# Performance work log

Measured on AMD Instinct MI355X. Metric: run time of the kernel, lower is better.

Reference implementation:

```python
import jax, jax.numpy as jnp
import numpy as np

L, H, E, DK, FF, V, BS = 6, 16, 1024, 64, 4096, 32000, 1024
B, T = 2, 1024
EPS = 1e-5


def _ln(x, g, b):
    mu = jnp.mean(x, axis=-1, keepdims=True)
    var = jnp.mean(jnp.square(x - mu), axis=-1, keepdims=True)
    return (x - mu) * jax.lax.rsqrt(var + EPS) * g + b


def setup_inputs() -> dict:
    key = jax.random.key(0)
    ks = jax.random.split(key, 12)
    s = 0.02
    return {
        'idx': jax.random.randint(ks[0], (B, T), 0, V),
        'emb': jax.random.normal(ks[1], (V, E), jnp.float32) * s,
        'pos': jax.random.normal(ks[2], (BS, E), jnp.float32) * s,
        'Wq': jax.random.normal(ks[3], (L, H, E, DK), jnp.float32) * s,
        'Wk': jax.random.normal(ks[4], (L, H, E, DK), jnp.float32) * s,
        'Wv': jax.random.normal(ks[5], (L, H, E, DK), jnp.float32) * s,
        'Wp': jax.random.normal(ks[6], (L, E, E), jnp.float32) * s,
        'bp': jnp.zeros((L, E), jnp.float32),
        'ln1_g': jnp.ones((L, E), jnp.float32),
        'ln1_b': jnp.zeros((L, E), jnp.float32),
        'ln2_g': jnp.ones((L, E), jnp.float32),
        'ln2_b': jnp.zeros((L, E), jnp.float32),
        'W1': jax.random.normal(ks[7], (L, E, FF), jnp.float32) * s,
        'b1': jnp.zeros((L, FF), jnp.float32),
        'W2': jax.random.normal(ks[8], (L, FF, E), jnp.float32) * s,
        'b2': jnp.zeros((L, E), jnp.float32),
        'lnf_g': jnp.ones((E,), jnp.float32),
        'lnf_b': jnp.zeros((E,), jnp.float32),
        'Wout': jax.random.normal(ks[9], (E, V), jnp.float32) * s,
        'bout': jnp.zeros((V,), jnp.float32),
    }


def reference(idx, emb, pos, Wq, Wk, Wv, Wp, bp, ln1_g, ln1_b, ln2_g, ln2_b,
              W1, b1, W2, b2, lnf_g, lnf_b, Wout, bout):
    Tcur = idx.shape[1]
    x = emb[idx] + pos[:Tcur]  # [B,T,E]
    # NOTE: original code scales by 1/sqrt(n_embd) (input dim), NOT 1/sqrt(d_k)
    scale = 1.0 / jnp.sqrt(jnp.float32(E))
    causal = jnp.tril(jnp.ones((Tcur, Tcur), bool))
    neg_inf = jnp.float32(-jnp.inf)
    for l in range(L):
        h = _ln(x, ln1_g[l], ln1_b[l])
        q = jnp.einsum('bte,hed->bhtd', h, Wq[l])
        k = jnp.einsum('bte,hed->bhtd', h, Wk[l])
        v = jnp.einsum('bte,hed->bhtd', h, Wv[l])
        scores = jnp.einsum('bhtd,bhsd->bhts', q, k) * scale
        scores = jnp.where(causal, scores, neg_inf)
        attn = jax.nn.softmax(scores, axis=-1)
        o = jnp.einsum('bhts,bhsd->bhtd', attn, v)
        o = o.transpose(0, 2, 1, 3).reshape(x.shape[0], Tcur, H * DK)
        x = x + o @ Wp[l] + bp[l]
        h = _ln(x, ln2_g[l], ln2_b[l])
        x = x + jax.nn.relu(h @ W1[l] + b1[l]) @ W2[l] + b2[l]
    x = _ln(x, lnf_g, lnf_b)
    logits = x @ Wout + bout  # [B,T,V]
    return logits
```

## Files before the change

### kernel.cpp

```cpp
#include <hip/hip_runtime.h>
#include <cstdio>
#include <cstdint>

typedef unsigned short u16;
typedef __bf16 bf16x8 __attribute__((ext_vector_type(8)));
typedef float f32x4 __attribute__((ext_vector_type(4)));

static const int EE = 1024;
static const int TT = 1024;
static const int BB = 2;
static const int NTOK = 2048;
static const int HH = 16;
static const int DK = 64;
static const int FF = 4096;
static const int VV = 32000;
static const int LL = 6;

__device__ __forceinline__ float bf2f(u16 u) {
  unsigned int i = ((unsigned int)u) << 16;
  float f; __builtin_memcpy(&f, &i, 4); return f;
}
__device__ __forceinline__ u16 f2bf(float f) {
  unsigned int i; __builtin_memcpy(&i, &f, 4);
  unsigned int r = i + 0x7fffu + ((i >> 16) & 1u);
  return (u16)(r >> 16);
}

__device__ __forceinline__ void gll16(const u16* g, u16* l) {
  __builtin_amdgcn_global_load_lds(
      (__attribute__((address_space(1))) void*)(uintptr_t)g,
      (__attribute__((address_space(3))) void*)l,
      16, 0, 0);
}

__global__ __launch_bounds__(256) void embed_k(const int* __restrict__ idx,
                                               const float* __restrict__ emb,
                                               const float* __restrict__ pos,
                                               float* __restrict__ x) {
  long i = (long)blockIdx.x * 256 + threadIdx.x;
  int n = (int)(i >> 10), e = (int)(i & 1023);
  int tok = idx[n];
  int t = n & (TT - 1);
  x[i] = emb[(long)tok * EE + e] + pos[(long)t * EE + e];
}

template <int NS>
__global__ __launch_bounds__(256) void ln_fused_k(float* __restrict__ x,
                                                  const float* __restrict__ part, long pstride,
                                                  const float* __restrict__ bias,
                                                  const float* __restrict__ g,
                                                  const float* __restrict__ b,
                                                  u16* __restrict__ out) {
  int row = blockIdx.x * 4 + (threadIdx.x >> 6);
  int lane = threadIdx.x & 63;
  long base = (long)row * EE;
  float v[16];
  float s = 0.f, s2 = 0.f;
#pragma unroll
  for (int j = 0; j < 16; j++) {
    int c = j * 64 + lane;
    float t = x[base + c];
    if constexpr (NS > 0) {
      t += bias[c];
#pragma unroll
      for (int p = 0; p < NS; p++) t += part[(long)p * pstride + base + c];
      x[base + c] = t;
    }
    v[j] = t; s += t; s2 += t * t;
  }
#pragma unroll
  for (int o = 32; o; o >>= 1) { s += __shfl_xor(s, o); s2 += __shfl_xor(s2, o); }
  float mu = s * (1.f / EE);
  float var = s2 * (1.f / EE) - mu * mu;
  float rs = rsqrtf(var + 1e-5f);
  u16* orow = out + base;
#pragma unroll
  for (int j = 0; j < 16; j++) {
    int c = j * 64 + lane;
    orow[c] = f2bf((v[j] - mu) * rs * g[c] + b[c]);
  }
}

__global__ __launch_bounds__(256) void pack_qkvT_k(const float* __restrict__ Wq,
                                                   const float* __restrict__ Wk,
                                                   const float* __restrict__ Wv,
                                                   u16* __restrict__ out) {
  int l = blockIdx.y;
  const float* Wq_l = Wq + (size_t)l * HH * EE * DK;
  const float* Wk_l = Wk + (size_t)l * HH * EE * DK;
  const float* Wv_l = Wv + (size_t)l * HH * EE * DK;
  u16* out_l = out + (size_t)l * 3 * EE * EE;
  long base = ((long)blockIdx.x * 256 + threadIdx.x) * 4;
  int c = (int)(base >> 10);
  int e0 = (int)(base & 1023);
  const float* W = (c < 1024) ? Wq_l : (c < 2048 ? Wk_l : Wv_l);
  int cm = c & 1023;
  int hh = cm >> 6, d = cm & 63;
#pragma unroll
  for (int i = 0; i < 4; i++) {
    int e = e0 + i;
    out_l[(long)c * EE + e] = f2bf(W[((long)hh * EE + e) * DK + d]);
  }
}

template <typename ST>
__global__ __launch_bounds__(256) void transpose_to_bf16(const ST* __restrict__ src,
                                                         long s_z1, long s_z2, int zmod, int ld_s,
                                                         u16* __restrict__ dst,
                                                         long d_z, int ld_d, int R, int C) {
  __shared__ u16 t[32][33];
  int z = blockIdx.z;
  const ST* S = src + (z / zmod) * s_z1 + (z % zmod) * s_z2;
  u16* D = dst + (long)z * d_z;
  int c0 = blockIdx.x * 32, r0 = blockIdx.y * 32;
  int lx = threadIdx.x & 31, ly = threadIdx.x >> 5;
#pragma unroll
  for (int i = 0; i < 4; i++) {
    int r = r0 + ly + i * 8;
    ST val = S[(long)r * ld_s + c0 + lx];
    if constexpr (sizeof(ST) == 4) t[ly + i * 8][lx] = f2bf((float)val);
    else t[ly + i * 8][lx] = (u16)val;
  }
  __syncthreads();
#pragma unroll
  for (int i = 0; i < 4; i++) {
    int c = c0 + ly + i * 8;
    D[(long)c * ld_d + r0 + lx] = t[lx][ly + i * 8];
  }
}

__global__ __launch_bounds__(256) void flash_attn_k(const u16* __restrict__ qkv,
                                                    const u16* __restrict__ vT,
                                                    u16* __restrict__ o) {
  __shared__ u16 Qs[64 * 72];
  __shared__ u16 Ks[2][64 * 72];
  __shared__ u16 Vs[2][64 * 72];
  __shared__ u16 Ps[4][16 * 72];

  int tid = threadIdx.x;
  int lane = tid & 63, w = tid >> 6;
  int fr = lane & 15, kg = lane >> 4;
  int z = blockIdx.y;
  int b = z >> 4, h = z & 15;
  const u16* qbase = qkv + (long)b * TT * 3072 + h * 64;
  const u16* kbase = qbase + 1024;
  const u16* vbase = vT + (long)z * DK * TT;
  const float scale = 0.03125f;

  for (int p = 0; p < 2; p++) {
    int jq = (p == 0) ? (int)blockIdx.x : 15 - (int)blockIdx.x;
    int q0 = jq * 64;
    int nt = jq + 1;
    if (p) __syncthreads();

    int4 kreg[2], vreg[2];
#pragma unroll
    for (int i = 0; i < 2; i++) {
      int c = i * 256 + tid, row = c >> 3, c8 = c & 7;
      *(int4*)&Qs[row * 72 + c8 * 8] = *(const int4*)(qbase + (long)(q0 + row) * 3072 + c8 * 8);
      kreg[i] = *(const int4*)(kbase + (long)row * 3072 + c8 * 8);
      vreg[i] = *(const int4*)(vbase + (long)row * TT + c8 * 8);
    }
#pragma unroll
    for (int i = 0; i < 2; i++) {
      int c = i * 256 + tid, row = c >> 3, c8 = c & 7;
      *(int4*)&Ks[0][row * 72 + c8 * 8] = kreg[i];
      *(int4*)&Vs[0][row * 72 + c8 * 8] = vreg[i];
    }
    __syncthreads();

    f32x4 zero = {0.f, 0.f, 0.f, 0.f};
    f32x4 acc_o[4];
    float m_i[4], l_i[4];
#pragma unroll
    for (int n = 0; n < 4; n++) acc_o[n] = zero;
#pragma unroll
    for (int r = 0; r < 4; r++) { m_i[r] = -1e30f; l_i[r] = 0.f; }

    for (int t = 0; t < nt; t++) {
      int cur = t & 1;
      int kv0 = t * 64;
      bool pf = (t + 1 < nt);
      if (pf) {
        int kvn = kv0 + 64;
#pragma unroll
        for (int i = 0; i < 2; i++) {
          int c = i * 256 + tid, row = c >> 3, c8 = c & 7;
          kreg[i] = *(const int4*)(kbase + (long)(kvn + row) * 3072 + c8 * 8);
          vreg[i] = *(const int4*)(vbase + (long)row * TT + kvn + c8 * 8);
        }
      }

      f32x4 s[4];
#pragma unroll
      for (int n = 0; n < 4; n++) s[n] = zero;
      {
        bf16x8 aq[2], bk[4][2];
#pragma unroll
        for (int kk = 0; kk < 2; kk++)
          aq[kk] = *(const bf16x8*)&Qs[(w * 16 + fr) * 72 + kk * 32 + kg * 8];
#pragma unroll
        for (int n = 0; n < 4; n++)
#pragma unroll
          for (int kk = 0; kk < 2; kk++)
            bk[n][kk] = *(const bf16x8*)&Ks[cur][(n * 16 + fr) * 72 + kk * 32 + kg * 8];
#pragma unroll
        for (int kk = 0; kk < 2; kk++)
#pragma unroll
          for (int n = 0; n < 4; n++)
            s[n] = __builtin_amdgcn_mfma_f32_16x16x32_bf16(aq[kk], bk[n][kk], s[n], 0, 0, 0);
      }

      float sv[4][4];
#pragma unroll
      for (int n = 0; n < 4; n++)
#pragma unroll
        for (int r = 0; r < 4; r++) {
          int qg = q0 + w * 16 + kg * 4 + r;
          int kgl = kv0 + n * 16 + fr;
          float val = s[n][r] * scale;
          sv[n][r] = (kgl > qg) ? -1e30f : val;
        }
#pragma unroll
      for (int r = 0; r < 4; r++) {
        float rm = fmaxf(fmaxf(sv[0][r], sv[1][r]), fmaxf(sv[2][r], sv[3][r]));
        rm = fmaxf(rm, __shfl_xor(rm, 1));
        rm = fmaxf(rm, __shfl_xor(rm, 2));
        rm = fmaxf(rm, __shfl_xor(rm, 4));
        rm = fmaxf(rm, __shfl_xor(rm, 8));
        float mn = fmaxf(m_i[r], rm);
        float f = __expf(m_i[r] - mn);
        m_i[r] = mn;
        float rs = 0.f;
#pragma unroll
        for (int n = 0; n < 4; n++) {
          float pv = __expf(sv[n][r] - mn);
          sv[n][r] = pv;
          rs += pv;
        }
        rs += __shfl_xor(rs, 1);
        rs += __shfl_xor(rs, 2);
        rs += __shfl_xor(rs, 4);
        rs += __shfl_xor(rs, 8);
        l_i[r] = l_i[r] * f + rs;
#pragma unroll
        for (int n = 0; n < 4; n++) acc_o[n][r] *= f;
      }
#pragma unroll
      for (int n = 0; n < 4; n++)
#pragma unroll
        for (int r = 0; r < 4; r++)
          Ps[w][(kg * 4 + r) * 72 + n * 16 + fr] = f2bf(sv[n][r]);

      {
        bf16x8 pa[2], bv[4][2];
#pragma unroll
        for (int kk = 0; kk < 2; kk++)
          pa[kk] = *(const bf16x8*)&Ps[w][fr * 72 + kk * 32 + kg * 8];
#pragma unroll
        for (int n = 0; n < 4; n++)
#pragma unroll
          for (int kk = 0; kk < 2; kk++)
            bv[n][kk] = *(const bf16x8*)&Vs[cur][(n * 16 + fr) * 72 + kk * 32 + kg * 8];
#pragma unroll
        for (int kk = 0; kk < 2; kk++)
#pragma unroll
          for (int n = 0; n < 4; n++)
            acc_o[n] = __builtin_amdgcn_mfma_f32_16x16x32_bf16(pa[kk], bv[n][kk], acc_o[n], 0, 0, 0);
      }

      if (pf) {
#pragma unroll
        for (int i = 0; i < 2; i++) {
          int c = i * 256 + tid, row = c >> 3, c8 = c & 7;
          *(int4*)&Ks[cur ^ 1][row * 72 + c8 * 8] = kreg[i];
          *(int4*)&Vs[cur ^ 1][row * 72 + c8 * 8] = vreg[i];
        }
      }
      __syncthreads();
    }

    u16* obase = o + ((long)b * TT + q0) * EE + h * 64;
#pragma unroll
    for (int r = 0; r < 4; r++) {
      float inv = 1.f / l_i[r];
      int qrow = w * 16 + kg * 4 + r;
#pragma unroll
      for (int n = 0; n < 4; n++)
        obase[(long)qrow * EE + n * 16 + fr] = f2bf(acc_o[n][r] * inv);
    }
  }
}

template <int EPI>
__global__ __launch_bounds__(256) void gemm_nt(
    const u16* __restrict__ A, const u16* __restrict__ BT, void* Cv,
    const float* __restrict__ bias,
    int Kc, int lda, int ldb, int ldc, long c_zs) {
  constexpr int BK = 64;
  __shared__ u16 As[128 * BK];
  __shared__ u16 Bs[128 * BK];

  int m0 = blockIdx.x * 128, n0 = blockIdx.y * 128;
  int z = blockIdx.z;
  int tid = threadIdx.x, lane = tid & 63, wave = tid >> 6;
  int wm = wave >> 1, wn = wave & 1;
  int fr = lane & 15, kg = lane >> 4;
  int xk0 = ((kg) ^ (fr & 7)) * 8;
  int xk1 = ((4 + kg) ^ (fr & 7)) * 8;

  f32x4 zero = {0.f, 0.f, 0.f, 0.f};
  f32x4 acc[4][4];
#pragma unroll
  for (int m = 0; m < 4; m++)
#pragma unroll
    for (int n = 0; n < 4; n++) acc[m][n] = zero;

  int kbeg = z * Kc;
  for (int k0 = kbeg; k0 < kbeg + Kc; k0 += BK) {
#pragma unroll
    for (int i = 0; i < 4; i++) {
      int c = i * 256 + tid, row = c >> 3;
      int ch = (c & 7) ^ (row & 7);
      gll16(A + (long)(m0 + row) * lda + k0 + ch * 8, &As[c * 8]);
      gll16(BT + (long)(n0 + row) * ldb + k0 + ch * 8, &Bs[c * 8]);
    }
    __syncthreads();
#pragma unroll
    for (int kk = 0; kk < 2; kk++) {
      int xo = kk ? xk1 : xk0;
      bf16x8 af[4], bf[4];
#pragma unroll
      for (int m = 0; m < 4; m++)
        af[m] = *(const bf16x8*)&As[(wm * 64 + m * 16 + fr) * BK + xo];
#pragma unroll
      for (int n = 0; n < 4; n++)
        bf[n] = *(const bf16x8*)&Bs[(wn * 64 + n * 16 + fr) * BK + xo];
#pragma unroll
      for (int m = 0; m < 4; m++)
#pragma unroll
        for (int n = 0; n < 4; n++)
          acc[m][n] = __builtin_amdgcn_mfma_f32_16x16x32_bf16(af[m], bf[n], acc[m][n], 0, 0, 0);
    }
    __syncthreads();
  }

  u16* C16 = (u16*)Cv;
  float* C32 = (float*)Cv;
  long cb = (long)z * c_zs;
  int rowb = m0 + wm * 64, colb = n0 + wn * 64;
#pragma unroll
  for (int m = 0; m < 4; m++) {
#pragma unroll
    for (int n = 0; n < 4; n++) {
      int gc = colb + n * 16 + fr;
      float bv = 0.f;
      if (EPI == 1 || EPI == 2) bv = bias[gc];
#pragma unroll
      for (int r = 0; r < 4; r++) {
        int gr = rowb + m * 16 + kg * 4 + r;
        long ci = cb + (long)gr * ldc + gc;
        float val = acc[m][n][r];
        if (EPI == 0) C16[ci] = f2bf(val);
        else if (EPI == 1) C32[ci] = val + bv;
        else if (EPI == 2) C16[ci] = f2bf(fmaxf(val + bv, 0.f));
        else C32[ci] = val;
      }
    }
  }
}

__global__ __launch_bounds__(512) void gemm256_nt(
    const u16* __restrict__ A, const u16* __restrict__ BT,
    float* __restrict__ C, const float* __restrict__ bias,
    int K, int lda, int ldb, int ldc) {
  __shared__ u16 lds[2][2][256 * 64];

  int tid = threadIdx.x, lane = tid & 63, wave = tid >> 6;
  int wm = wave >> 2, wn = wave & 3;
  int fr = lane & 15, kg = lane >> 4;
  int m0 = blockIdx.x * 256, n0 = blockIdx.y * 256;

  auto STAGE = [&](int t, int b) {
    int k0 = t * 64;
#pragma unroll
    for (int r = 0; r < 4; r++) {
      int g = r * 512 + tid;
      int row = g >> 3, cl = (g & 7) ^ (row & 7);
      gll16(A + (long)(m0 + row) * lda + k0 + cl * 8, &lds[b][0][g * 8]);
    }
#pragma unroll
    for (int r = 0; r < 4; r++) {
      int g = r * 512 + tid;
      int row = g >> 3, cl = (g & 7) ^ (row & 7);
      gll16(BT + (long)(n0 + row) * ldb + k0 + cl * 8, &lds[b][1][g * 8]);
    }
  };

  f32x4 zero = {0.f, 0.f, 0.f, 0.f};
  f32x4 acc[8][4];
#pragma unroll
  for (int m = 0; m < 8; m++)
#pragma unroll
    for (int n = 0; n < 4; n++) acc[m][n] = zero;

  int NT = K / 64;
  STAGE(0, 0);
  if (NT > 1) STAGE(1, 1);

  for (int c = 0; c < NT; c++) {
    if (c + 1 < NT) asm volatile("s_waitcnt vmcnt(8)" ::: "memory");
    else            asm volatile("s_waitcnt vmcnt(0)" ::: "memory");
    __builtin_amdgcn_s_barrier();
    const u16* Ab = lds[c & 1][0];
    const u16* Bb = lds[c & 1][1];
#pragma unroll
    for (int ph = 0; ph < 4; ph++) {
      int mh = ph >> 1, nh = ph & 1;
      bf16x8 af[4][2], bf[2][2];
#pragma unroll
      for (int m = 0; m < 4; m++) {
        int row = wm * 128 + mh * 64 + m * 16 + fr;
#pragma unroll
        for (int kk = 0; kk < 2; kk++) {
          int cp = (kk * 4 + kg) ^ (row & 7);
          af[m][kk] = *(const bf16x8*)&Ab[row * 64 + cp * 8];
        }
      }
#pragma unroll
      for (int n = 0; n < 2; n++) {
        int row = wn * 64 + nh * 32 + n * 16 + fr;
#pragma unroll
        for (int kk = 0; kk < 2; kk++) {
          int cp = (kk * 4 + kg) ^ (row & 7);
          bf[n][kk] = *(const bf16x8*)&Bb[row * 64 + cp * 8];
        }
      }
      __builtin_amdgcn_s_setprio(1);
#pragma unroll
      for (int kk = 0; kk < 2; kk++)
#pragma unroll
        for (int m = 0; m < 4; m++)
#pragma unroll
          for (int n = 0; n < 2; n++)
            acc[mh * 4 + m][nh * 2 + n] = __builtin_amdgcn_mfma_f32_16x16x32_bf16(
                af[m][kk], bf[n][kk], acc[mh * 4 + m][nh * 2 + n], 0, 0, 0);
      __builtin_amdgcn_s_setprio(0);
    }
    __builtin_amdgcn_s_barrier();
    if (c + 2 < NT) STAGE(c + 2, c & 1);
  }

  int rowb = m0 + wm * 128, colb = n0 + wn * 64;
#pragma unroll
  for (int m = 0; m < 8; m++) {
#pragma unroll
    for (int n = 0; n < 4; n++) {
      int gc = colb + n * 16 + fr;
      float bv = bias[gc];
#pragma unroll
      for (int r = 0; r < 4; r++) {
        int gr = rowb + m * 16 + kg * 4 + r;
        C[(long)gr * ldc + gc] = acc[m][n][r] + bv;
      }
    }
  }
}

extern "C" void kernel_launch(void* const* d_in, const int* in_sizes, int n_in,
                              void* d_out, int out_size, void* d_ws, size_t ws_size,
                              hipStream_t stream) {
  const int*   idx  = (const int*)d_in[0];
  const float* emb  = (const float*)d_in[1];
  const float* pos  = (const float*)d_in[2];
  const float* Wq   = (const float*)d_in[3];
  const float* Wk   = (const float*)d_in[4];
  const float* Wv   = (const float*)d_in[5];
  const float* Wp   = (const float*)d_in[6];
  const float* bp   = (const float*)d_in[7];
  const float* ln1g = (const float*)d_in[8];
  const float* ln1b = (const float*)d_in[9];
  const float* ln2g = (const float*)d_in[10];
  const float* ln2b = (const float*)d_in[11];
  const float* W1   = (const float*)d_in[12];
  const float* b1   = (const float*)d_in[13];
  const float* W2   = (const float*)d_in[14];
  const float* b2   = (const float*)d_in[15];
  const float* lnfg = (const float*)d_in[16];
  const float* lnfb = (const float*)d_in[17];
  const float* Wout = (const float*)d_in[18];
  const float* bout = (const float*)d_in[19];

  char* w = (char*)d_ws;
  size_t off = 0;
  auto alloc = [&](size_t bytes) {
    void* p = w + off;
    off += (bytes + 255) & ~(size_t)255;
    return p;
  };
  float* x    = (float*)alloc((size_t)NTOK * EE * 4);
  u16* h      = (u16*)alloc((size_t)NTOK * EE * 2);
  u16* qkv    = (u16*)alloc((size_t)NTOK * 3 * EE * 2);
  u16* vT     = (u16*)alloc((size_t)BB * HH * DK * TT * 2);
  u16* big    = (u16*)alloc((size_t)VV * EE * 2);
  u16* o      = (u16*)alloc((size_t)NTOK * EE * 2);
  u16* mid    = (u16*)alloc((size_t)NTOK * FF * 2);
  u16* W1T    = (u16*)alloc((size_t)FF * EE * 2);
  u16* W2T    = (u16*)alloc((size_t)EE * FF * 2);
  float* pbuf = (float*)alloc((size_t)4 * NTOK * EE * 4);
  if (off > ws_size) {
    fprintf(stderr, "kernel_launch: ws too small, need %zu have %zu\n", off, ws_size);
    return;
  }
  u16* WqkvT_all = big;
  u16* WpT_all   = big + (size_t)6 * 3 * EE * EE;
  const long PS = (long)NTOK * EE;

  embed_k<<<NTOK * EE / 256, 256, 0, stream>>>(idx, emb, pos, x);
  pack_qkvT_k<<<dim3(3 * EE * EE / 1024, LL), 256, 0, stream>>>(Wq, Wk, Wv, WqkvT_all);
  transpose_to_bf16<float><<<dim3(32, 32, LL), 256, 0, stream>>>(
      Wp, (long)EE * EE, 0, 1, EE, WpT_all, (long)EE * EE, EE, EE, EE);

  for (int l = 0; l < LL; l++) {
    if (l == 0)
      ln_fused_k<0><<<NTOK / 4, 256, 0, stream>>>(x, nullptr, 0, nullptr,
                                                  ln1g, ln1b, h);
    else
      ln_fused_k<4><<<NTOK / 4, 256, 0, stream>>>(x, pbuf, PS, b2 + (l - 1) * EE,
                                                  ln1g + l * EE, ln1b + l * EE, h);
    gemm_nt<0><<<dim3(16, 24, 1), 256, 0, stream>>>(
        h, WqkvT_all + (size_t)l * 3 * EE * EE, qkv, nullptr,
        EE, EE, EE, 3 * EE, 0);
    transpose_to_bf16<u16><<<dim3(2, 32, 32), 256, 0, stream>>>(
        qkv + 2 * EE, (long)TT * 3 * EE, 64, 16, 3 * EE,
        vT, (long)DK * TT, TT, TT, DK);
    flash_attn_k<<<dim3(8, 32), 256, 0, stream>>>(qkv, vT, o);
    gemm_nt<4><<<dim3(16, 8, 2), 256, 0, stream>>>(
        o, WpT_all + (size_t)l * EE * EE, pbuf, nullptr,
        512, EE, EE, EE, PS);
    ln_fused_k<2><<<NTOK / 4, 256, 0, stream>>>(x, pbuf, PS, bp + l * EE,
                                                ln2g + l * EE, ln2b + l * EE, h);
    transpose_to_bf16<float><<<dim3(FF / 32, EE / 32, 1), 256, 0, stream>>>(
        W1 + (size_t)l * EE * FF, 0, 0, 1, FF, W1T, 0, EE, EE, FF);
    gemm_nt<2><<<dim3(16, 32, 1), 256, 0, stream>>>(
        h, W1T, mid, b1 + l * FF,
        EE, EE, EE, FF, 0);
    transpose_to_bf16<float><<<dim3(EE / 32, FF / 32, 1), 256, 0, stream>>>(
        W2 + (size_t)l * FF * EE, 0, 0, 1, EE, W2T, 0, FF, FF, EE);
    gemm_nt<4><<<dim3(16, 8, 4), 256, 0, stream>>>(
        mid, W2T, pbuf, nullptr,
        1024, FF, FF, EE, PS);
  }

  ln_fused_k<4><<<NTOK / 4, 256, 0, stream>>>(x, pbuf, PS, b2 + 5 * EE, lnfg, lnfb, h);
  u16* WoutT = big;
  transpose_to_bf16<float><<<dim3(VV / 32, EE / 32, 1), 256, 0, stream>>>(
      Wout, 0, 0, 1, VV, WoutT, 0, EE, EE, VV);
  gemm256_nt<<<dim3(NTOK / 256, VV / 256, 1), 512, 0, stream>>>(
      h, WoutT, (float*)d_out, bout, EE, EE, EE, VV);
}
```

Before: 1.383 ms.

## Restructure vocab GEMM into 8-phase loop with quarter-tile staggered prefetch

The final 256x256 logits GEMM now unrolls two K-tiles into eight phases per iteration and splits each global-to-LDS stage into quarter loads issued one per phase. The intent is to interleave global loads, LDS reads and MFMA work more finely so memory latency hides behind compute, instead of issuing a whole stage after a barrier. It adds one barrier per phase and precomputed swizzle offsets. The risks are more synchronisation overhead and reliance on exact vmcnt accounting for correctness.

```diff
diff --git a/kernel.cpp b/kernel.cpp
--- a/kernel.cpp
+++ b/kernel.cpp
@@ -370,7 +370,7 @@
   }
 }
 
-__global__ __launch_bounds__(512) void gemm256_nt(
+__global__ __launch_bounds__(512) void gemm256_8ph(
     const u16* __restrict__ A, const u16* __restrict__ BT,
     float* __restrict__ C, const float* __restrict__ bias,
     int K, int lda, int ldb, int ldc) {
@@ -380,20 +380,22 @@
   int wm = wave >> 2, wn = wave & 3;
   int fr = lane & 15, kg = lane >> 4;
   int m0 = blockIdx.x * 256, n0 = blockIdx.y * 256;
-
-  auto STAGE = [&](int t, int b) {
+  int xk0 = ((kg) ^ (fr & 7)) * 8;
+  int xk1 = ((4 + kg) ^ (fr & 7)) * 8;
+
+  auto STAGEQ = [&](int t, int b, int q) {
     int k0 = t * 64;
-#pragma unroll
-    for (int r = 0; r < 4; r++) {
+    int op = q >> 1, half = q & 1;
+    const u16* src = op ? BT : A;
+    int ld = op ? ldb : lda;
+    int gbase = op ? n0 : m0;
+#pragma unroll
+    for (int r = 0; r < 2; r++) {
       int g = r * 512 + tid;
-      int row = g >> 3, cl = (g & 7) ^ (row & 7);
-      gll16(A + (long)(m0 + row) * lda + k0 + cl * 8, &lds[b][0][g * 8]);
-    }
-#pragma unroll
-    for (int r = 0; r < 4; r++) {
-      int g = r * 512 + tid;
-      int row = g >> 3, cl = (g & 7) ^ (row & 7);
-      gll16(BT + (long)(n0 + row) * ldb + k0 + cl * 8, &lds[b][1][g * 8]);
+      int row = g >> 3, c8 = g & 7;
+      int cl = c8 ^ (row & 7);
+      gll16(src + (long)(gbase + half * 128 + row) * ld + k0 + cl * 8,
+            &lds[b][op][(half * 128 + row) * 64 + c8 * 8]);
     }
   };
 
@@ -405,37 +407,60 @@
     for (int n = 0; n < 4; n++) acc[m][n] = zero;
 
   int NT = K / 64;
-  STAGE(0, 0);
-  if (NT > 1) STAGE(1, 1);
-
-  for (int c = 0; c < NT; c++) {
-    if (c + 1 < NT) asm volatile("s_waitcnt vmcnt(8)" ::: "memory");
-    else            asm volatile("s_waitcnt vmcnt(0)" ::: "memory");
-    __builtin_amdgcn_s_barrier();
-    const u16* Ab = lds[c & 1][0];
-    const u16* Bb = lds[c & 1][1];
-#pragma unroll
-    for (int ph = 0; ph < 4; ph++) {
-      int mh = ph >> 1, nh = ph & 1;
-      bf16x8 af[4][2], bf[2][2];
-#pragma unroll
-      for (int m = 0; m < 4; m++) {
-        int row = wm * 128 + mh * 64 + m * 16 + fr;
-#pragma unroll
-        for (int kk = 0; kk < 2; kk++) {
-          int cp = (kk * 4 + kg) ^ (row & 7);
-          af[m][kk] = *(const bf16x8*)&Ab[row * 64 + cp * 8];
-        }
-      }
-#pragma unroll
-      for (int n = 0; n < 2; n++) {
-        int row = wn * 64 + nh * 32 + n * 16 + fr;
-#pragma unroll
-        for (int kk = 0; kk < 2; kk++) {
-          int cp = (kk * 4 + kg) ^ (row & 7);
-          bf[n][kk] = *(const bf16x8*)&Bb[row * 64 + cp * 8];
-        }
-      }
+  int NJ = NT / 2;
+  STAGEQ(0, 0, 0); STAGEQ(0, 0, 1); STAGEQ(0, 0, 2); STAGEQ(0, 0, 3);
+
+  for (int j = 0; j < NJ; j++) {
+#pragma unroll
+    for (int p = 0; p < 8; p++) {
+      const int kt = p >> 2;
+      const int q = p & 3;
+      const int mh = q >> 1, nh = q & 1;
+      int st = kt ? (2 * j + 2) : (2 * j + 1);
+      int sb = kt ? 0 : 1;
+      bool issue = (st < NT);
+      const u16* Ab = lds[kt][0];
+      const u16* Bb = lds[kt][1];
+      bf16x8 af[4][2], bfr[2][2];
+
+      if (q == 0) {
+        if (issue) {
+          STAGEQ(st, sb, 0);
+          asm volatile("s_waitcnt vmcnt(2)" ::: "memory");
+        } else {
+          asm volatile("s_waitcnt vmcnt(0)" ::: "memory");
+        }
+        __builtin_amdgcn_s_barrier();
+#pragma unroll
+        for (int m = 0; m < 4; m++) {
+          int row = wm * 128 + mh * 64 + m * 16 + fr;
+          af[m][0] = *(const bf16x8*)&Ab[row * 64 + xk0];
+          af[m][1] = *(const bf16x8*)&Ab[row * 64 + xk1];
+        }
+#pragma unroll
+        for (int n = 0; n < 2; n++) {
+          int row = wn * 64 + nh * 32 + n * 16 + fr;
+          bfr[n][0] = *(const bf16x8*)&Bb[row * 64 + xk0];
+          bfr[n][1] = *(const bf16x8*)&Bb[row * 64 + xk1];
+        }
+      } else {
+#pragma unroll
+        for (int m = 0; m < 4; m++) {
+          int row = wm * 128 + mh * 64 + m * 16 + fr;
+          af[m][0] = *(const bf16x8*)&Ab[row * 64 + xk0];
+          af[m][1] = *(const bf16x8*)&Ab[row * 64 + xk1];
+        }
+#pragma unroll
+        for (int n = 0; n < 2; n++) {
+          int row = wn * 64 + nh * 32 + n * 16 + fr;
+          bfr[n][0] = *(const bf16x8*)&Bb[row * 64 + xk0];
+          bfr[n][1] = *(const bf16x8*)&Bb[row * 64 + xk1];
+        }
+        if (issue) STAGEQ(st, sb, q);
+        __builtin_amdgcn_s_barrier();
+      }
+      asm volatile("s_waitcnt lgkmcnt(0)" ::: "memory");
+      __builtin_amdgcn_sched_barrier(0);
       __builtin_amdgcn_s_setprio(1);
 #pragma unroll
       for (int kk = 0; kk < 2; kk++)
@@ -444,11 +469,10 @@
 #pragma unroll
           for (int n = 0; n < 2; n++)
             acc[mh * 4 + m][nh * 2 + n] = __builtin_amdgcn_mfma_f32_16x16x32_bf16(
-                af[m][kk], bf[n][kk], acc[mh * 4 + m][nh * 2 + n], 0, 0, 0);
+                af[m][kk], bfr[n][kk], acc[mh * 4 + m][nh * 2 + n], 0, 0, 0);
       __builtin_amdgcn_s_setprio(0);
-    }
-    __builtin_amdgcn_s_barrier();
-    if (c + 2 < NT) STAGE(c + 2, c & 1);
+      __builtin_amdgcn_s_barrier();
+    }
   }
 
   int rowb = m0 + wm * 128, colb = n0 + wn * 64;
@@ -556,6 +580,6 @@
   u16* WoutT = big;
   transpose_to_bf16<float><<<dim3(VV / 32, EE / 32, 1), 256, 0, stream>>>(
       Wout, 0, 0, 1, VV, WoutT, 0, EE, EE, VV);
-  gemm256_nt<<<dim3(NTOK / 256, VV / 256, 1), 512, 0, stream>>>(
+  gemm256_8ph<<<dim3(NTOK / 256, VV / 256, 1), 512, 0, stream>>>(
       h, WoutT, (float*)d_out, bout, EE, EE, EE, VV);
 }
```

After: 1.387 ms. Within noise of the previous version (+0.3%).

## Double-buffer LDS in gemm_nt with async global loads and nontemporal logits stores

Applied to the files above, without the earlier changes.

Converts the generic gemm_nt kernel from single-buffered LDS with full syncthreads to a two-stage double buffer. The next K tile's global-to-LDS loads are issued while the current tile is computed, with waits done through vmcnt counts and raw barriers, and MFMA priority is raised during the compute phase. The output-projection GEMM also writes logits with nontemporal stores to reduce cache pollution. The cost is double the LDS per block, which may lower occupancy.

```diff
diff --git a/kernel.cpp b/kernel.cpp
--- a/kernel.cpp
+++ b/kernel.cpp
@@ -298,8 +298,8 @@
     const float* __restrict__ bias,
     int Kc, int lda, int ldb, int ldc, long c_zs) {
   constexpr int BK = 64;
-  __shared__ u16 As[128 * BK];
-  __shared__ u16 Bs[128 * BK];
+  __shared__ u16 As[2][128 * BK];
+  __shared__ u16 Bs[2][128 * BK];
 
   int m0 = blockIdx.x * 128, n0 = blockIdx.y * 128;
   int z = blockIdx.z;
@@ -308,41 +308,56 @@
   int fr = lane & 15, kg = lane >> 4;
   int xk0 = ((kg) ^ (fr & 7)) * 8;
   int xk1 = ((4 + kg) ^ (fr & 7)) * 8;
-
-  f32x4 zero = {0.f, 0.f, 0.f, 0.f};
-  f32x4 acc[4][4];
-#pragma unroll
-  for (int m = 0; m < 4; m++)
-#pragma unroll
-    for (int n = 0; n < 4; n++) acc[m][n] = zero;
-
   int kbeg = z * Kc;
-  for (int k0 = kbeg; k0 < kbeg + Kc; k0 += BK) {
+
+  auto STAGE = [&](int t, int b) {
+    int k0 = kbeg + t * BK;
 #pragma unroll
     for (int i = 0; i < 4; i++) {
       int c = i * 256 + tid, row = c >> 3;
       int ch = (c & 7) ^ (row & 7);
-      gll16(A + (long)(m0 + row) * lda + k0 + ch * 8, &As[c * 8]);
-      gll16(BT + (long)(n0 + row) * ldb + k0 + ch * 8, &Bs[c * 8]);
-    }
-    __syncthreads();
+      gll16(A + (long)(m0 + row) * lda + k0 + ch * 8, &As[b][c * 8]);
+      gll16(BT + (long)(n0 + row) * ldb + k0 + ch * 8, &Bs[b][c * 8]);
+    }
+  };
+
+  f32x4 zero = {0.f, 0.f, 0.f, 0.f};
+  f32x4 acc[4][4];
+#pragma unroll
+  for (int m = 0; m < 4; m++)
+#pragma unroll
+    for (int n = 0; n < 4; n++) acc[m][n] = zero;
+
+  int NT = Kc / BK;
+  STAGE(0, 0);
+  if (NT > 1) STAGE(1, 1);
+
+  for (int c = 0; c < NT; c++) {
+    if (c + 1 < NT) asm volatile("s_waitcnt vmcnt(8)" ::: "memory");
+    else            asm volatile("s_waitcnt vmcnt(0)" ::: "memory");
+    __builtin_amdgcn_s_barrier();
+    const u16* Ab = As[c & 1];
+    const u16* Bb = Bs[c & 1];
 #pragma unroll
     for (int kk = 0; kk < 2; kk++) {
       int xo = kk ? xk1 : xk0;
       bf16x8 af[4], bf[4];
 #pragma unroll
       for (int m = 0; m < 4; m++)
-        af[m] = *(const bf16x8*)&As[(wm * 64 + m * 16 + fr) * BK + xo];
+        af[m] = *(const bf16x8*)&Ab[(wm * 64 + m * 16 + fr) * BK + xo];
 #pragma unroll
       for (int n = 0; n < 4; n++)
-        bf[n] = *(const bf16x8*)&Bs[(wn * 64 + n * 16 + fr) * BK + xo];
+        bf[n] = *(const bf16x8*)&Bb[(wn * 64 + n * 16 + fr) * BK + xo];
+      __builtin_amdgcn_s_setprio(1);
 #pragma unroll
       for (int m = 0; m < 4; m++)
 #pragma unroll
         for (int n = 0; n < 4; n++)
           acc[m][n] = __builtin_amdgcn_mfma_f32_16x16x32_bf16(af[m], bf[n], acc[m][n], 0, 0, 0);
-    }
-    __syncthreads();
+      __builtin_amdgcn_s_setprio(0);
+    }
+    __builtin_amdgcn_s_barrier();
+    if (c + 2 < NT) STAGE(c + 2, c & 1);
   }
 
   u16* C16 = (u16*)Cv;
@@ -461,7 +476,7 @@
 #pragma unroll
       for (int r = 0; r < 4; r++) {
         int gr = rowb + m * 16 + kg * 4 + r;
-        C[(long)gr * ldc + gc] = acc[m][n][r] + bv;
+        __builtin_nontemporal_store(acc[m][n][r] + bv, &C[(long)gr * ldc + gc]);
       }
     }
   }
```

New measurement: 1.338 ms. -3.3%, faster.
